# Kernel optimization log

Hardware: AMD Instinct MI355X
Metric: run time of the kernel (lower is better)

The kernel has to match this reference:

```python
import jax, jax.numpy as jnp
import numpy as np

B, T, E, H = 8, 2048, 1024, 64

def setup_inputs() -> dict:
    key = jax.random.key(0)
    k1, k2, k3, k4 = jax.random.split(key, 4)
    x = jax.random.normal(k1, (B, T, E), dtype=jnp.float32)
    # Linear(E, H, bias=False) weights stored as [E, H] (x @ W)
    s = 1.0 / np.sqrt(E)
    Wk = jax.random.normal(k2, (E, H), dtype=jnp.float32) * s
    Wq = jax.random.normal(k3, (E, H), dtype=jnp.float32) * s
    Wv = jax.random.normal(k4, (E, H), dtype=jnp.float32) * s
    return {"x": x, "Wk": Wk, "Wq": Wq, "Wv": Wv}

def reference(x, Wk, Wq, Wv):
    _, t, e = x.shape
    k = jnp.einsum('bte,eh->bth', x, Wk)
    q = jnp.einsum('bte,eh->bth', x, Wq)
    v = jnp.einsum('bte,eh->bth', x, Wv)
    # NOTE: original scales by E**-0.5 (embedding dim), not head_size**-0.5
    wei = jnp.einsum('bqh,bkh->bqk', q, k) * (e ** -0.5)
    causal = jnp.tril(jnp.ones((t, t), dtype=bool))
    wei = jnp.where(causal, wei, -jnp.inf)
    wei = jax.nn.softmax(wei, axis=-1)
    out = jnp.einsum('bqk,bkh->bqh', wei, v)
    return out
```

## Files before the change

kernel.cpp:

```cpp
#include <hip/hip_runtime.h>

typedef unsigned short u16;
typedef unsigned int u32;
typedef __bf16 bf16x8 __attribute__((ext_vector_type(8)));
typedef __bf16 bf16x4 __attribute__((ext_vector_type(4)));
typedef float f32x4 __attribute__((ext_vector_type(4)));

constexpr int Bn = 8, Tn = 2048, En = 1024, Hn = 64;
constexpr int Mrows = Bn * Tn;
constexpr float CEXP = 0.03125f * 1.4426950408889634f;

__device__ __forceinline__ u16 f2bf(float f) {
  u32 u = __float_as_uint(f);
  return (u16)((u + 0x7fffu + ((u >> 16) & 1u)) >> 16);
}

__global__ __launch_bounds__(256) void wt_kernel(
    const float* __restrict__ Wk, const float* __restrict__ Wq,
    const float* __restrict__ Wv, u16* __restrict__ Wt) {
  __shared__ u16 tile[64][72];
  const int mat = blockIdx.x >> 4;
  const int k0 = (blockIdx.x & 15) * 64;
  const float* W = (mat == 0) ? Wk : (mat == 1) ? Wq : Wv;
  const int t = threadIdx.x;
  {
    const int kl = t >> 2;
    const int h0 = (t & 3) * 16;
    const float4* src = (const float4*)(W + (size_t)(k0 + kl) * Hn + h0);
#pragma unroll
    for (int i = 0; i < 4; ++i) {
      float4 v = src[i];
      tile[h0 + 4 * i + 0][kl] = f2bf(v.x);
      tile[h0 + 4 * i + 1][kl] = f2bf(v.y);
      tile[h0 + 4 * i + 2][kl] = f2bf(v.z);
      tile[h0 + 4 * i + 3][kl] = f2bf(v.w);
    }
  }
  __syncthreads();
  {
    const int hl = t >> 2;
    const int kk = (t & 3) * 16;
    uint4 a = *(const uint4*)&tile[hl][kk];
    uint4 b = *(const uint4*)&tile[hl][kk + 8];
    u16* dst = Wt + (size_t)mat * Hn * En + (size_t)hl * En + k0 + kk;
    *(uint4*)dst = a;
    *(uint4*)(dst + 8) = b;
  }
}

__global__ __launch_bounds__(256, 2) void qkv_kernel(
    const float* __restrict__ x, const u16* __restrict__ Wt,
    u16* __restrict__ Kb16, u16* __restrict__ Qb16, u16* __restrict__ Vt16) {
  constexpr int NR = 32, BK = 64, LDK = BK + 8;
  __shared__ u16 xs[NR * LDK];
  const int t = threadIdx.x;
  const int w = t >> 6, lane = t & 63;
  const int quad = lane >> 4, l16 = lane & 15;
  const int r0 = blockIdx.x * NR;

  const int srow = t >> 3, schunk = t & 7;
  const float* xp = x + (size_t)(r0 + srow) * En + schunk * 8;
  u16* xsw = xs + srow * LDK + schunk * 8;

  const u16* wpb = Wt + (size_t)l16 * En + quad * 8;

  f32x4 acc[3][2];
#pragma unroll
  for (int i = 0; i < 3; ++i)
#pragma unroll
    for (int nt = 0; nt < 2; ++nt) acc[i][nt] = (f32x4){0.f, 0.f, 0.f, 0.f};

  float4 pre0 = *(const float4*)(xp);
  float4 pre1 = *(const float4*)(xp + 4);

  for (int k0 = 0; k0 < En; k0 += BK) {
    __syncthreads();
    {
      bf16x8 pk;
      pk[0] = (__bf16)pre0.x; pk[1] = (__bf16)pre0.y;
      pk[2] = (__bf16)pre0.z; pk[3] = (__bf16)pre0.w;
      pk[4] = (__bf16)pre1.x; pk[5] = (__bf16)pre1.y;
      pk[6] = (__bf16)pre1.z; pk[7] = (__bf16)pre1.w;
      *(bf16x8*)xsw = pk;
    }
    __syncthreads();
    if (k0 + BK < En) {
      pre0 = *(const float4*)(xp + k0 + BK);
      pre1 = *(const float4*)(xp + k0 + BK + 4);
    }
#pragma unroll
    for (int ks = 0; ks < 2; ++ks) {
      bf16x8 b0 = *(const bf16x8*)(xs + l16 * LDK + ks * 32 + quad * 8);
      bf16x8 b1 = *(const bf16x8*)(xs + (16 + l16) * LDK + ks * 32 + quad * 8);
#pragma unroll
      for (int i = 0; i < 3; ++i) {
        const int mt = 3 * w + i;
        bf16x8 a = *(const bf16x8*)(wpb + (size_t)(mt * 16) * En + k0 + ks * 32);
        acc[i][0] = __builtin_amdgcn_mfma_f32_16x16x32_bf16(a, b0, acc[i][0], 0, 0, 0);
        acc[i][1] = __builtin_amdgcn_mfma_f32_16x16x32_bf16(a, b1, acc[i][1], 0, 0, 0);
      }
    }
  }

#pragma unroll
  for (int i = 0; i < 3; ++i) {
    const int mt = 3 * w + i;
    const int mat = mt >> 2, ht = mt & 3;
#pragma unroll
    for (int nt = 0; nt < 2; ++nt) {
      const int row = r0 + nt * 16 + l16;
      f32x4 a = acc[i][nt];
      if (mat < 2) {
        u16* dst = ((mat == 0) ? Kb16 : Qb16) + (size_t)row * Hn + ht * 16 + quad * 4;
        uint2 pk;
        pk.x = (u32)f2bf(a[0]) | ((u32)f2bf(a[1]) << 16);
        pk.y = (u32)f2bf(a[2]) | ((u32)f2bf(a[3]) << 16);
        *(uint2*)dst = pk;
      } else {
        const int bb = row >> 11, tt = row & 2047;
        u16* base = Vt16 + ((size_t)bb * 64) * Tn + tt;
#pragma unroll
        for (int r = 0; r < 4; ++r)
          base[(size_t)(ht * 16 + quad * 4 + r) * Tn] = f2bf(a[r]);
      }
    }
  }
}

__global__ __launch_bounds__(256, 4) void attn_kernel(
    const u16* __restrict__ Qb16, const u16* __restrict__ Kb16,
    const u16* __restrict__ Vt16, float* __restrict__ out) {
  __shared__ u16 pt[2][4][16][40];
  __shared__ float l_sh[4][16];
  __shared__ float o_sh[4][16][68];

  const int idx = blockIdx.x;
  const int b = idx & 7;
  const int tq = 127 - (idx >> 3);
  const int w = threadIdx.x >> 6, lane = threadIdx.x & 63;
  const int quad = lane >> 4, l16 = lane & 15;
  const int qbase = tq * 16;
  const int limit = qbase + 16;
  const int ch = ((limit + 127) >> 7) << 5;
  const int lo = w * ch;
  const int hi = min(lo + ch, limit);
  const int q_abs = qbase + l16;

  const u16* Kp = Kb16 + (size_t)b * Tn * Hn;
  const u16* Vp = Vt16 + (size_t)b * 64 * Tn;

  const u16* qrow = Qb16 + ((size_t)b * Tn + q_abs) * Hn + quad * 8;
  const bf16x8 qb0 = *(const bf16x8*)(qrow);
  const bf16x8 qb1 = *(const bf16x8*)(qrow + 32);

  f32x4 od0 = {0.f, 0.f, 0.f, 0.f}, od1 = od0, od2 = od0, od3 = od0;
  f32x4 lacc = {0.f, 0.f, 0.f, 0.f};

#pragma unroll 2
  for (int kb = lo; kb < hi; kb += 32) {
    const int par = (kb >> 5) & 1;
    const u16* krow0 = Kp + (size_t)(kb + l16) * Hn + quad * 8;
    const u16* krow1 = krow0 + (size_t)16 * Hn;
    f32x4 z = {0.f, 0.f, 0.f, 0.f};
    f32x4 st0 = __builtin_amdgcn_mfma_f32_16x16x32_bf16(*(const bf16x8*)(krow0), qb0, z, 0, 0, 0);
    st0 = __builtin_amdgcn_mfma_f32_16x16x32_bf16(*(const bf16x8*)(krow0 + 32), qb1, st0, 0, 0, 0);
    f32x4 st1 = __builtin_amdgcn_mfma_f32_16x16x32_bf16(*(const bf16x8*)(krow1), qb0, z, 0, 0, 0);
    st1 = __builtin_amdgcn_mfma_f32_16x16x32_bf16(*(const bf16x8*)(krow1 + 32), qb1, st1, 0, 0, 0);

    if (kb + 15 > qbase) {
#pragma unroll
      for (int r = 0; r < 4; ++r)
        if (kb + quad * 4 + r > q_abs) st0[r] = -3.0e38f;
    }
    if (kb + 31 > qbase) {
#pragma unroll
      for (int r = 0; r < 4; ++r)
        if (kb + 16 + quad * 4 + r > q_abs) st1[r] = -3.0e38f;
    }

    f32x4 p0, p1;
#pragma unroll
    for (int r = 0; r < 4; ++r) {
      p0[r] = __builtin_amdgcn_exp2f(st0[r] * CEXP);
      p1[r] = __builtin_amdgcn_exp2f(st1[r] * CEXP);
    }
    lacc += p0;
    lacc += p1;

    {
      bf16x4 w0, w1;
      w0[0] = (__bf16)p0[0]; w0[1] = (__bf16)p0[1];
      w0[2] = (__bf16)p0[2]; w0[3] = (__bf16)p0[3];
      w1[0] = (__bf16)p1[0]; w1[1] = (__bf16)p1[1];
      w1[2] = (__bf16)p1[2]; w1[3] = (__bf16)p1[3];
      *(bf16x4*)&pt[par][w][l16][quad * 4] = w0;
      *(bf16x4*)&pt[par][w][l16][16 + quad * 4] = w1;
    }
    const bf16x8 pb = *(const bf16x8*)&pt[par][w][l16][quad * 8];

    const u16* vrow = Vp + (size_t)l16 * Tn + kb + quad * 8;
    od0 = __builtin_amdgcn_mfma_f32_16x16x32_bf16(*(const bf16x8*)(vrow), pb, od0, 0, 0, 0);
    od1 = __builtin_amdgcn_mfma_f32_16x16x32_bf16(*(const bf16x8*)(vrow + (size_t)16 * Tn), pb, od1, 0, 0, 0);
    od2 = __builtin_amdgcn_mfma_f32_16x16x32_bf16(*(const bf16x8*)(vrow + (size_t)32 * Tn), pb, od2, 0, 0, 0);
    od3 = __builtin_amdgcn_mfma_f32_16x16x32_bf16(*(const bf16x8*)(vrow + (size_t)48 * Tn), pb, od3, 0, 0, 0);
  }

  float l = (lacc[0] + lacc[1]) + (lacc[2] + lacc[3]);
  l += __shfl_xor(l, 16);
  l += __shfl_xor(l, 32);
  if (quad == 0) l_sh[w][l16] = l;
  *(f32x4*)&o_sh[w][l16][0 * 16 + quad * 4] = od0;
  *(f32x4*)&o_sh[w][l16][1 * 16 + quad * 4] = od1;
  *(f32x4*)&o_sh[w][l16][2 * 16 + quad * 4] = od2;
  *(f32x4*)&o_sh[w][l16][3 * 16 + quad * 4] = od3;
  __syncthreads();

  const int qq = threadIdx.x >> 4, dq = threadIdx.x & 15;
  float lg = 0.f;
  f32x4 acc = {0.f, 0.f, 0.f, 0.f};
#pragma unroll
  for (int ww = 0; ww < 4; ++ww) {
    lg += l_sh[ww][qq];
    acc += *(const f32x4*)&o_sh[ww][qq][dq * 4];
  }
  acc *= (1.f / lg);
  *(f32x4*)(out + ((size_t)b * Tn + qbase + qq) * Hn + dq * 4) = acc;
}

extern "C" void kernel_launch(void* const* d_in, const int* in_sizes, int n_in,
                              void* d_out, int out_size, void* d_ws, size_t ws_size,
                              hipStream_t stream) {
  const void* x = nullptr;
  const void* Ws[3] = {nullptr, nullptr, nullptr};
  int wj = 0;
  for (int i = 0; i < n_in; ++i) {
    if (in_sizes[i] == Bn * Tn * En) x = d_in[i];
    else if (wj < 3) Ws[wj++] = d_in[i];
  }
  const float* Wk = (const float*)Ws[0];
  const float* Wq = (const float*)Ws[1];
  const float* Wv = (const float*)Ws[2];

  u16* Kb16 = (u16*)d_ws;
  u16* Qb16 = Kb16 + (size_t)Mrows * Hn;
  u16* Vt16 = Qb16 + (size_t)Mrows * Hn;
  u16* Wt   = Vt16 + (size_t)Mrows * Hn;

  wt_kernel<<<48, 256, 0, stream>>>(Wk, Wq, Wv, Wt);
  qkv_kernel<<<Mrows / 32, 256, 0, stream>>>((const float*)x, Wt, Kb16, Qb16, Vt16);
  attn_kernel<<<Bn * (Tn / 16), 256, 0, stream>>>(Qb16, Kb16, Vt16, (float*)d_out);
}
```

Before: 158.9 us.

## Split long causal query tiles across multiple blocks with a combine pass

The attention kernel now splits the key range of each 16-row query tile into 512-key chunks handled by separate blocks. Tiles near the end of the sequence get up to 4 blocks, which evens out work per block and raises the block count from 1024 to 2560. Partial unnormalized outputs and row sums go to workspace, and a new combine kernel adds them and normalizes. This relies on exp without max subtraction, so the partials can simply be summed. The cost is an extra launch plus the global traffic for writing and reading the partials.

```diff
diff --git a/kernel.cpp b/kernel.cpp
--- a/kernel.cpp
+++ b/kernel.cpp
@@ -9,6 +9,7 @@
 constexpr int Bn = 8, Tn = 2048, En = 1024, Hn = 64;
 constexpr int Mrows = Bn * Tn;
 constexpr float CEXP = 0.03125f * 1.4426950408889634f;
+constexpr int RPB = 320;
 
 __device__ __forceinline__ u16 f2bf(float f) {
   u32 u = __float_as_uint(f);
@@ -127,23 +128,29 @@
   }
 }
 
-__global__ __launch_bounds__(256, 4) void attn_kernel(
+__global__ __launch_bounds__(256, 4) void attn_partial(
     const u16* __restrict__ Qb16, const u16* __restrict__ Kb16,
-    const u16* __restrict__ Vt16, float* __restrict__ out) {
+    const u16* __restrict__ Vt16, float* __restrict__ Po,
+    float* __restrict__ Pl, float* __restrict__ out) {
   __shared__ u16 pt[2][4][16][40];
   __shared__ float l_sh[4][16];
   __shared__ float o_sh[4][16][68];
 
   const int idx = blockIdx.x;
   const int b = idx & 7;
-  const int tq = 127 - (idx >> 3);
+  const int r = idx >> 3;
+  int tq, c, n;
+  if (r < 128)      { tq = 96 + (r >> 2); c = r & 3; n = 4; }
+  else if (r < 224) { const int s = r - 128; const int d = s / 3; tq = 64 + d; c = s - d * 3; n = 3; }
+  else if (r < 288) { const int s = r - 224; tq = 32 + (s >> 1); c = s & 1; n = 2; }
+  else              { tq = r - 288; c = 0; n = 1; }
+
   const int w = threadIdx.x >> 6, lane = threadIdx.x & 63;
   const int quad = lane >> 4, l16 = lane & 15;
   const int qbase = tq * 16;
   const int limit = qbase + 16;
-  const int ch = ((limit + 127) >> 7) << 5;
-  const int lo = w * ch;
-  const int hi = min(lo + ch, limit);
+  const int lo = c * 512 + w * 128;
+  const int hi = min(lo + 128, limit);
   const int q_abs = qbase + l16;
 
   const u16* Kp = Kb16 + (size_t)b * Tn * Hn;
@@ -169,20 +176,20 @@
 
     if (kb + 15 > qbase) {
 #pragma unroll
-      for (int r = 0; r < 4; ++r)
-        if (kb + quad * 4 + r > q_abs) st0[r] = -3.0e38f;
+      for (int rr = 0; rr < 4; ++rr)
+        if (kb + quad * 4 + rr > q_abs) st0[rr] = -3.0e38f;
     }
     if (kb + 31 > qbase) {
 #pragma unroll
-      for (int r = 0; r < 4; ++r)
-        if (kb + 16 + quad * 4 + r > q_abs) st1[r] = -3.0e38f;
+      for (int rr = 0; rr < 4; ++rr)
+        if (kb + 16 + quad * 4 + rr > q_abs) st1[rr] = -3.0e38f;
     }
 
     f32x4 p0, p1;
 #pragma unroll
-    for (int r = 0; r < 4; ++r) {
-      p0[r] = __builtin_amdgcn_exp2f(st0[r] * CEXP);
-      p1[r] = __builtin_amdgcn_exp2f(st1[r] * CEXP);
+    for (int rr = 0; rr < 4; ++rr) {
+      p0[rr] = __builtin_amdgcn_exp2f(st0[rr] * CEXP);
+      p1[rr] = __builtin_amdgcn_exp2f(st1[rr] * CEXP);
     }
     lacc += p0;
     lacc += p1;
@@ -223,8 +230,35 @@
     lg += l_sh[ww][qq];
     acc += *(const f32x4*)&o_sh[ww][qq][dq * 4];
   }
+  if (n == 1) {
+    acc *= (1.f / lg);
+    *(f32x4*)(out + ((size_t)b * Tn + qbase + qq) * Hn + dq * 4) = acc;
+  } else {
+    *(f32x4*)(Po + ((size_t)idx * 16 + qq) * Hn + dq * 4) = acc;
+    if (dq == 0) Pl[(size_t)idx * 16 + qq] = lg;
+  }
+}
+
+__global__ __launch_bounds__(256) void attn_combine(
+    const float* __restrict__ Po, const float* __restrict__ Pl,
+    float* __restrict__ out) {
+  const int idx = blockIdx.x;
+  const int b = idx & 7;
+  const int tq = 32 + (idx >> 3);
+  int r0, n;
+  if (tq >= 96)      { r0 = (tq - 96) * 4; n = 4; }
+  else if (tq >= 64) { r0 = 128 + (tq - 64) * 3; n = 3; }
+  else               { r0 = 224 + (tq - 32) * 2; n = 2; }
+  const int qq = threadIdx.x >> 4, dq = threadIdx.x & 15;
+  float lg = 0.f;
+  f32x4 acc = {0.f, 0.f, 0.f, 0.f};
+  for (int j = 0; j < n; ++j) {
+    const int pid = (r0 + j) * 8 + b;
+    lg += Pl[(size_t)pid * 16 + qq];
+    acc += *(const f32x4*)(Po + ((size_t)pid * 16 + qq) * Hn + dq * 4);
+  }
   acc *= (1.f / lg);
-  *(f32x4*)(out + ((size_t)b * Tn + qbase + qq) * Hn + dq * 4) = acc;
+  *(f32x4*)(out + ((size_t)b * Tn + tq * 16 + qq) * Hn + dq * 4) = acc;
 }
 
 extern "C" void kernel_launch(void* const* d_in, const int* in_sizes, int n_in,
@@ -245,8 +279,11 @@
   u16* Qb16 = Kb16 + (size_t)Mrows * Hn;
   u16* Vt16 = Qb16 + (size_t)Mrows * Hn;
   u16* Wt   = Vt16 + (size_t)Mrows * Hn;
+  float* Po = (float*)(Wt + 3 * Hn * En);
+  float* Pl = Po + (size_t)(Bn * RPB) * 16 * Hn;
 
   wt_kernel<<<48, 256, 0, stream>>>(Wk, Wq, Wv, Wt);
   qkv_kernel<<<Mrows / 32, 256, 0, stream>>>((const float*)x, Wt, Kb16, Qb16, Vt16);
-  attn_kernel<<<Bn * (Tn / 16), 256, 0, stream>>>(Qb16, Kb16, Vt16, (float*)d_out);
-}
+  attn_partial<<<Bn * RPB, 256, 0, stream>>>(Qb16, Kb16, Vt16, Po, Pl, (float*)d_out);
+  attn_combine<<<Bn * 96, 256, 0, stream>>>(Po, Pl, (float*)d_out);
+}
```

Result: slower. 166.0 us (+4.4%).
